# Optimization experiments

Hardware: AMD Instinct MI355X
Metric: run time of the kernel (lower is better)

Reference implementation:

```python
import jax, jax.numpy as jnp
import numpy as np

V, D, H, KV, L, FF, HD = 32000, 768, 12, 4, 4, 2048, 64
N_REP = H // KV  # 3
EPS = 1e-6
ROPE_THETA = 10000.0


def setup_inputs() -> dict:
    key = jax.random.key(0)
    ks = jax.random.split(key, 12)
    s = 0.02
    return {
        'idx': jax.random.randint(ks[0], (1, 2048), 0, V),
        'embed': jax.random.normal(ks[1], (V, D), jnp.float32) * s,
        'ln1_w': jnp.ones((L, D), jnp.float32),
        'Wq': jax.random.normal(ks[2], (L, D, H * HD), jnp.float32) * s,
        'Wk': jax.random.normal(ks[3], (L, D, KV * HD), jnp.float32) * s,
        'Wv': jax.random.normal(ks[4], (L, D, KV * HD), jnp.float32) * s,
        'Wo': jax.random.normal(ks[5], (L, H * HD, D), jnp.float32) * s,
        'ln2_w': jnp.ones((L, D), jnp.float32),
        'Wg': jax.random.normal(ks[6], (L, D, FF), jnp.float32) * s,
        'Wu': jax.random.normal(ks[7], (L, D, FF), jnp.float32) * s,
        'Wd': jax.random.normal(ks[8], (L, FF, D), jnp.float32) * s,
        'normf_w': jnp.ones((D,), jnp.float32),
    }


def _rms(x, w):
    xf = x.astype(jnp.float32)
    var = jnp.mean(xf * xf, axis=-1, keepdims=True)
    return w * (xf * jax.lax.rsqrt(var + EPS)).astype(x.dtype)


def _rotate_half(x):
    x1, x2 = x[..., : x.shape[-1] // 2], x[..., x.shape[-1] // 2:]
    return jnp.concatenate((-x2, x1), axis=-1)


def reference(idx, embed, ln1_w, Wq, Wk, Wv, Wo, ln2_w, Wg, Wu, Wd, normf_w):
    B, T = idx.shape
    x = embed[idx]  # [B,T,D]

    # RoPE tables: cos/sin [1,1,T,HD]
    inv_freq = 1.0 / (ROPE_THETA ** (jnp.arange(0, HD, 2, dtype=jnp.float32) / HD))
    pos = jnp.arange(T, dtype=jnp.float32)
    freqs = pos[:, None] * inv_freq[None, :]          # [T,HD/2]
    emb = jnp.concatenate((freqs, freqs), axis=-1)     # [T,HD]
    cos = jnp.cos(emb)[None, None].astype(x.dtype)
    sin = jnp.sin(emb)[None, None].astype(x.dtype)

    causal = jnp.tril(jnp.ones((T, T), bool))[None, None]  # [1,1,T,T]
    scale = 1.0 / np.sqrt(HD)

    for l in range(L):
        # --- attention ---
        h = _rms(x, ln1_w[l])
        q = (h @ Wq[l]).reshape(B, T, H, HD).transpose(0, 2, 1, 3)   # [B,H,T,HD]
        k = (h @ Wk[l]).reshape(B, T, KV, HD).transpose(0, 2, 1, 3)  # [B,KV,T,HD]
        v = (h @ Wv[l]).reshape(B, T, KV, HD).transpose(0, 2, 1, 3)
        q = q * cos + _rotate_half(q) * sin
        k = k * cos + _rotate_half(k) * sin
        k = jnp.repeat(k, N_REP, axis=1)  # [B,H,T,HD]
        v = jnp.repeat(v, N_REP, axis=1)
        scores = jnp.einsum('bhqd,bhkd->bhqk', q, k) * scale
        scores = jnp.where(causal, scores, -jnp.inf)
        probs = jax.nn.softmax(scores.astype(jnp.float32), axis=-1).astype(q.dtype)
        attn = jnp.einsum('bhqk,bhkd->bhqd', probs, v)
        attn = attn.transpose(0, 2, 1, 3).reshape(B, T, H * HD)
        x = x + attn @ Wo[l]
        # --- gated MLP ---
        h = _rms(x, ln2_w[l])
        x = x + (jax.nn.gelu(h @ Wg[l], approximate=True) * (h @ Wu[l])) @ Wd[l]

    x = _rms(x, normf_w)
    logits = (x @ embed.T).astype(jnp.float32)  # tied lm_head
    return logits
```

## Files before the change

### kernel.cpp

```cpp
#include <hip/hip_runtime.h>

#define TSEQ 2048
#define DM   768
#define NH   12
#define NKV  4
#define HD   64
#define FFD  2048
#define NL   4
#define VOC  32000
#define QKVN 1280

typedef __attribute__((ext_vector_type(8))) short short8;
typedef __attribute__((ext_vector_type(4))) float f32x4;

__device__ __forceinline__ unsigned short f2b(float f) {
  unsigned int u = __float_as_uint(f);
  u += 0x7fffu + ((u >> 16) & 1u);
  return (unsigned short)(u >> 16);
}
__device__ __forceinline__ float b2f(unsigned short u) {
  return __uint_as_float(((unsigned int)u) << 16);
}
__device__ __forceinline__ unsigned int packbf(float a, float b) {
  return (unsigned int)f2b(a) | ((unsigned int)f2b(b) << 16);
}

__device__ __forceinline__ void gl16(const unsigned short* g, unsigned short* l) {
  __builtin_amdgcn_global_load_lds(
      (const __attribute__((address_space(1))) void*)g,
      (__attribute__((address_space(3))) void*)l, 16, 0, 0);
}

__global__ void cast_bf16_kernel(const float* __restrict__ src,
                                 unsigned short* __restrict__ dst, int n4) {
  int i = blockIdx.x * blockDim.x + threadIdx.x;
  if (i >= n4) return;
  float4 v = ((const float4*)src)[i];
  uint2 o; o.x = packbf(v.x, v.y); o.y = packbf(v.z, v.w);
  ((uint2*)dst)[i] = o;
}

__global__ void rope_tab_kernel(float2* __restrict__ tab) {
  int i = blockIdx.x * blockDim.x + threadIdx.x;
  int pos = i >> 5, d = i & 31;
  float inv = exp2f(-(float)d * (13.287712379549449f / 32.0f));
  float sv, cv; sincosf((float)pos * inv, &sv, &cv);
  tab[i] = make_float2(cv, sv);
}

__global__ void transpose_cast_kernel(const float* __restrict__ src,
                                      unsigned short* __restrict__ dst,
                                      int K, int N, size_t sstride, size_t dstride) {
  __shared__ float tile[32][33];
  src += (size_t)blockIdx.z * sstride;
  dst += (size_t)blockIdx.z * dstride;
  int n0 = blockIdx.x * 32, k0 = blockIdx.y * 32;
  int tx = threadIdx.x, ty = threadIdx.y;
  #pragma unroll
  for (int i = 0; i < 4; ++i) {
    int r = ty + i * 8;
    tile[r][tx] = src[(size_t)(k0 + r) * N + n0 + tx];
  }
  __syncthreads();
  #pragma unroll
  for (int i = 0; i < 4; ++i) {
    int r = ty + i * 8;
    dst[(size_t)(n0 + r) * K + k0 + tx] = f2b(tile[tx][r]);
  }
}

__global__ void gather_kernel(const int* __restrict__ idx,
                              const float* __restrict__ embed,
                              float* __restrict__ x) {
  int row = blockIdx.x; int t = threadIdx.x;
  int id = idx[row];
  ((float4*)(x + (size_t)row * DM))[t] = ((const float4*)(embed + (size_t)id * DM))[t];
}

__global__ void rmsnorm_kernel(const float* __restrict__ x,
                               const float* __restrict__ w,
                               unsigned short* __restrict__ out) {
  int row = blockIdx.x; int t = threadIdx.x;
  const float* xr = x + (size_t)row * DM;
  float v0 = xr[t], v1 = xr[t + 256], v2 = xr[t + 512];
  float s = v0*v0 + v1*v1 + v2*v2;
  #pragma unroll
  for (int off = 1; off < 64; off <<= 1) s += __shfl_xor(s, off);
  __shared__ float red[4];
  if ((t & 63) == 0) red[t >> 6] = s;
  __syncthreads();
  float tot = red[0] + red[1] + red[2] + red[3];
  float rs = rsqrtf(tot * (1.0f / DM) + 1e-6f);
  unsigned short* orow = out + (size_t)row * DM;
  orow[t]       = f2b(w[t]       * v0 * rs);
  orow[t + 256] = f2b(w[t + 256] * v1 * rs);
  orow[t + 512] = f2b(w[t + 512] * v2 * rs);
}

__global__ __launch_bounds__(512, 1) void gemm_l8_kernel(
    const unsigned short* __restrict__ A, const unsigned short* __restrict__ Bt,
    float* __restrict__ C, int N, int K) {
  __shared__ unsigned short lds[2][2][256 * 64];
  const int NT = K >> 6;
  int bid = blockIdx.x, nwg = gridDim.x;
  int wgid = (bid & 7) * (nwg >> 3) + (bid >> 3);
  int m0 = (wgid & 7) * 256;
  int n0 = (wgid >> 3) * 256;
  int tid = threadIdx.x;
  int lane = tid & 63, w = tid >> 6;
  int wm = w >> 2, wn = w & 3;
  int al = lane & 15, ag = lane >> 4;
  int swz = (al & 7) << 3;

  int rA = tid >> 3;
  int cK = ((tid & 7) * 8) ^ ((rA & 7) << 3);
  const unsigned short* Ag = A + (size_t)(m0 + rA) * K + cK;
  const unsigned short* Bg = Bt + (size_t)(n0 + rA) * K + cK;

  f32x4 acc[8][4];
  #pragma unroll
  for (int i = 0; i < 8; ++i)
    #pragma unroll
    for (int n = 0; n < 4; ++n) acc[i][n] = (f32x4){0.f, 0.f, 0.f, 0.f};

  #define STAGE(kt, c) { \
    size_t ko = (size_t)(kt) * 64; \
    unsigned short* dA = &lds[(c)][0][0] + w * 512; \
    unsigned short* dB = &lds[(c)][1][0] + w * 512; \
    gl16(Ag + (size_t)0   * K + ko, dA);            \
    gl16(Ag + (size_t)64  * K + ko, dA + 4096);     \
    gl16(Ag + (size_t)128 * K + ko, dA + 8192);     \
    gl16(Ag + (size_t)192 * K + ko, dA + 12288);    \
    gl16(Bg + (size_t)0   * K + ko, dB);            \
    gl16(Bg + (size_t)64  * K + ko, dB + 4096);     \
    gl16(Bg + (size_t)128 * K + ko, dB + 8192);     \
    gl16(Bg + (size_t)192 * K + ko, dB + 12288);    \
  }

  STAGE(0, 0);
  STAGE(1, 1);
  asm volatile("s_waitcnt vmcnt(8)" ::: "memory");
  __builtin_amdgcn_s_barrier();

  for (int t = 0; t < NT; ++t) {
    int cur = t & 1;
    const unsigned short* La = &lds[cur][0][0];
    const unsigned short* Lb = &lds[cur][1][0];
    short8 a0[8], b0[4], a1[8], b1[4];
    #pragma unroll
    for (int i = 0; i < 8; ++i)
      a0[i] = *(const short8*)&La[(wm*128 + i*16 + al)*64 + ((ag*8) ^ swz)];
    #pragma unroll
    for (int n = 0; n < 4; ++n)
      b0[n] = *(const short8*)&Lb[(wn*64 + n*16 + al)*64 + ((ag*8) ^ swz)];
    #pragma unroll
    for (int i = 0; i < 8; ++i)
      #pragma unroll
      for (int n = 0; n < 4; ++n)
        acc[i][n] = __builtin_amdgcn_mfma_f32_16x16x32_bf16(a0[i], b0[n], acc[i][n], 0, 0, 0);
    #pragma unroll
    for (int i = 0; i < 8; ++i)
      a1[i] = *(const short8*)&La[(wm*128 + i*16 + al)*64 + ((32 + ag*8) ^ swz)];
    #pragma unroll
    for (int n = 0; n < 4; ++n)
      b1[n] = *(const short8*)&Lb[(wn*64 + n*16 + al)*64 + ((32 + ag*8) ^ swz)];
    asm volatile("s_waitcnt lgkmcnt(0)" ::: "memory");
    __builtin_amdgcn_s_barrier();
    if (t + 2 < NT) STAGE(t + 2, cur);
    __builtin_amdgcn_s_setprio(1);
    #pragma unroll
    for (int i = 0; i < 8; ++i)
      #pragma unroll
      for (int n = 0; n < 4; ++n)
        acc[i][n] = __builtin_amdgcn_mfma_f32_16x16x32_bf16(a1[i], b1[n], acc[i][n], 0, 0, 0);
    __builtin_amdgcn_s_setprio(0);
    if (t + 2 < NT) { asm volatile("s_waitcnt vmcnt(8)" ::: "memory"); }
    else            { asm volatile("s_waitcnt vmcnt(0)" ::: "memory"); }
    __builtin_amdgcn_s_barrier();
  }
  #undef STAGE

  #pragma unroll
  for (int i = 0; i < 8; ++i)
    #pragma unroll
    for (int r = 0; r < 4; ++r) {
      float* Cr = C + (size_t)(m0 + wm*128 + i*16 + ag*4 + r) * N + n0 + wn*64 + al;
      #pragma unroll
      for (int n = 0; n < 4; ++n) Cr[n * 16] = acc[i][n][r];
    }
}

__global__ __launch_bounds__(512) void gemm_p8_kernel(
    const unsigned short* __restrict__ A, const unsigned short* __restrict__ Bt,
    float* __restrict__ C, int N, int K, int Kc) {
  __shared__ unsigned short lds[2][2][128 * 64];
  const int NT = Kc >> 6;
  int bid = blockIdx.x, nwg = gridDim.x;
  int wgid = (bid & 7) * (nwg >> 3) + (bid >> 3);
  int m0 = (wgid & 15) * 128;
  int n0 = (wgid >> 4) * 128;
  int tid = threadIdx.x;
  int lane = tid & 63, w = tid >> 6;
  int wm = w >> 2, wn = w & 3;
  int al = lane & 15, ag = lane >> 4;
  int swz = (al & 7) << 3;

  size_t koff = (size_t)blockIdx.y * Kc;
  int rp = 8 * w + (lane >> 3);
  int cK = ((lane & 7) * 8) ^ ((lane >> 3) << 3);
  const unsigned short* Ag = A + (size_t)(m0 + rp) * K + koff + cK;
  const unsigned short* Bg = Bt + (size_t)(n0 + rp) * K + koff + cK;

  f32x4 acc[4][2];
  #pragma unroll
  for (int i = 0; i < 4; ++i)
    #pragma unroll
    for (int n = 0; n < 2; ++n) acc[i][n] = (f32x4){0.f, 0.f, 0.f, 0.f};

  #define STAGE(kt, c) { \
    size_t ko = (size_t)(kt) * 64; \
    unsigned short* dA = &lds[(c)][0][0] + w * 512; \
    unsigned short* dB = &lds[(c)][1][0] + w * 512; \
    gl16(Ag + ko,                 dA);        \
    gl16(Ag + (size_t)64*K + ko,  dA + 4096); \
    gl16(Bg + ko,                 dB);        \
    gl16(Bg + (size_t)64*K + ko,  dB + 4096); \
  }

  STAGE(0, 0);
  STAGE(1, 1);
  asm volatile("s_waitcnt vmcnt(4)" ::: "memory");
  __builtin_amdgcn_s_barrier();

  for (int t = 0; t < NT; ++t) {
    int cur = t & 1;
    const unsigned short* La = &lds[cur][0][0];
    const unsigned short* Lb = &lds[cur][1][0];
    short8 a0[4], b0[2], a1[4], b1[2];
    #pragma unroll
    for (int i = 0; i < 4; ++i)
      a0[i] = *(const short8*)&La[(wm*64 + i*16 + al)*64 + ((ag*8) ^ swz)];
    #pragma unroll
    for (int n = 0; n < 2; ++n)
      b0[n] = *(const short8*)&Lb[(wn*32 + n*16 + al)*64 + ((ag*8) ^ swz)];
    #pragma unroll
    for (int i = 0; i < 4; ++i)
      #pragma unroll
      for (int n = 0; n < 2; ++n)
        acc[i][n] = __builtin_amdgcn_mfma_f32_16x16x32_bf16(a0[i], b0[n], acc[i][n], 0, 0, 0);
    #pragma unroll
    for (int i = 0; i < 4; ++i)
      a1[i] = *(const short8*)&La[(wm*64 + i*16 + al)*64 + ((32 + ag*8) ^ swz)];
    #pragma unroll
    for (int n = 0; n < 2; ++n)
      b1[n] = *(const short8*)&Lb[(wn*32 + n*16 + al)*64 + ((32 + ag*8) ^ swz)];
    asm volatile("s_waitcnt lgkmcnt(0)" ::: "memory");
    __builtin_amdgcn_s_barrier();
    if (t + 2 < NT) STAGE(t + 2, cur);
    __builtin_amdgcn_s_setprio(1);
    #pragma unroll
    for (int i = 0; i < 4; ++i)
      #pragma unroll
      for (int n = 0; n < 2; ++n)
        acc[i][n] = __builtin_amdgcn_mfma_f32_16x16x32_bf16(a1[i], b1[n], acc[i][n], 0, 0, 0);
    __builtin_amdgcn_s_setprio(0);
    if (t + 2 < NT) { asm volatile("s_waitcnt vmcnt(4)" ::: "memory"); }
    else            { asm volatile("s_waitcnt vmcnt(0)" ::: "memory"); }
    __builtin_amdgcn_s_barrier();
  }
  #undef STAGE

  #pragma unroll
  for (int i = 0; i < 4; ++i)
    #pragma unroll
    for (int r = 0; r < 4; ++r) {
      float* Cr = C + (size_t)(m0 + wm*64 + i*16 + ag*4 + r) * N + n0 + wn*32 + al;
      #pragma unroll
      for (int n = 0; n < 2; ++n) atomicAdd(&Cr[n * 16], acc[i][n][r]);
    }
}

__device__ __forceinline__ float gelu_t(float x) {
  float x3 = x * x * x;
  return 0.5f * x * (1.0f + tanhf(0.7978845608028654f * (x + 0.044715f * x3)));
}

__global__ __launch_bounds__(512) void gemm_gu8_kernel(
    const unsigned short* __restrict__ A, const unsigned short* __restrict__ BtG,
    const unsigned short* __restrict__ BtU, unsigned short* __restrict__ Cm) {
  __shared__ unsigned short lds[2][3][128 * 64];
  const int K = DM;
  const int NT = K >> 6;
  int bid = blockIdx.x, nwg = gridDim.x;
  int wgid = (bid & 7) * (nwg >> 3) + (bid >> 3);
  int m0 = (wgid & 15) * 128;
  int n0 = (wgid >> 4) * 128;
  int tid = threadIdx.x;
  int lane = tid & 63, w = tid >> 6;
  int wm = w >> 2, wn = w & 3;
  int al = lane & 15, ag = lane >> 4;
  int swz = (al & 7) << 3;

  int rp = 8 * w + (lane >> 3);
  int cK = ((lane & 7) * 8) ^ ((lane >> 3) << 3);
  const unsigned short* Ag = A + (size_t)(m0 + rp) * K + cK;
  const unsigned short* Gg = BtG + (size_t)(n0 + rp) * K + cK;
  const unsigned short* Ug = BtU + (size_t)(n0 + rp) * K + cK;

  f32x4 accg[4][2], accu[4][2];
  #pragma unroll
  for (int i = 0; i < 4; ++i)
    #pragma unroll
    for (int n = 0; n < 2; ++n) {
      accg[i][n] = (f32x4){0.f, 0.f, 0.f, 0.f};
      accu[i][n] = (f32x4){0.f, 0.f, 0.f, 0.f};
    }

  #define STAGE(kt, c) { \
    size_t ko = (size_t)(kt) * 64; \
    unsigned short* dA = &lds[(c)][0][0] + w * 512; \
    unsigned short* dG = &lds[(c)][1][0] + w * 512; \
    unsigned short* dU = &lds[(c)][2][0] + w * 512; \
    gl16(Ag + ko,                 dA);        \
    gl16(Ag + (size_t)64*K + ko,  dA + 4096); \
    gl16(Gg + ko,                 dG);        \
    gl16(Gg + (size_t)64*K + ko,  dG + 4096); \
    gl16(Ug + ko,                 dU);        \
    gl16(Ug + (size_t)64*K + ko,  dU + 4096); \
  }

  STAGE(0, 0);
  STAGE(1, 1);
  asm volatile("s_waitcnt vmcnt(6)" ::: "memory");
  __builtin_amdgcn_s_barrier();

  for (int t = 0; t < NT; ++t) {
    int cur = t & 1;
    const unsigned short* La = &lds[cur][0][0];
    const unsigned short* Lg = &lds[cur][1][0];
    const unsigned short* Lu = &lds[cur][2][0];
    short8 a0[4], g0[2], u0[2], a1[4], g1[2], u1[2];
    #pragma unroll
    for (int i = 0; i < 4; ++i)
      a0[i] = *(const short8*)&La[(wm*64 + i*16 + al)*64 + ((ag*8) ^ swz)];
    #pragma unroll
    for (int n = 0; n < 2; ++n) {
      g0[n] = *(const short8*)&Lg[(wn*32 + n*16 + al)*64 + ((ag*8) ^ swz)];
      u0[n] = *(const short8*)&Lu[(wn*32 + n*16 + al)*64 + ((ag*8) ^ swz)];
    }
    #pragma unroll
    for (int i = 0; i < 4; ++i)
      #pragma unroll
      for (int n = 0; n < 2; ++n) {
        accg[i][n] = __builtin_amdgcn_mfma_f32_16x16x32_bf16(a0[i], g0[n], accg[i][n], 0, 0, 0);
        accu[i][n] = __builtin_amdgcn_mfma_f32_16x16x32_bf16(a0[i], u0[n], accu[i][n], 0, 0, 0);
      }
    #pragma unroll
    for (int i = 0; i < 4; ++i)
      a1[i] = *(const short8*)&La[(wm*64 + i*16 + al)*64 + ((32 + ag*8) ^ swz)];
    #pragma unroll
    for (int n = 0; n < 2; ++n) {
      g1[n] = *(const short8*)&Lg[(wn*32 + n*16 + al)*64 + ((32 + ag*8) ^ swz)];
      u1[n] = *(const short8*)&Lu[(wn*32 + n*16 + al)*64 + ((32 + ag*8) ^ swz)];
    }
    asm volatile("s_waitcnt lgkmcnt(0)" ::: "memory");
    __builtin_amdgcn_s_barrier();
    if (t + 2 < NT) STAGE(t + 2, cur);
    __builtin_amdgcn_s_setprio(1);
    #pragma unroll
    for (int i = 0; i < 4; ++i)
      #pragma unroll
      for (int n = 0; n < 2; ++n) {
        accg[i][n] = __builtin_amdgcn_mfma_f32_16x16x32_bf16(a1[i], g1[n], accg[i][n], 0, 0, 0);
        accu[i][n] = __builtin_amdgcn_mfma_f32_16x16x32_bf16(a1[i], u1[n], accu[i][n], 0, 0, 0);
      }
    __builtin_amdgcn_s_setprio(0);
    if (t + 2 < NT) { asm volatile("s_waitcnt vmcnt(6)" ::: "memory"); }
    else            { asm volatile("s_waitcnt vmcnt(0)" ::: "memory"); }
    __builtin_amdgcn_s_barrier();
  }
  #undef STAGE

  #pragma unroll
  for (int i = 0; i < 4; ++i)
    #pragma unroll
    for (int r = 0; r < 4; ++r) {
      unsigned short* Cr = Cm + (size_t)(m0 + wm*64 + i*16 + ag*4 + r) * FFD + n0 + wn*32 + al;
      #pragma unroll
      for (int n = 0; n < 2; ++n)
        Cr[n * 16] = f2b(gelu_t(accg[i][n][r]) * accu[i][n][r]);
    }
}

__global__ __launch_bounds__(256) void gemm_qkv_kernel(
    const unsigned short* __restrict__ A, const unsigned short* __restrict__ Bt,
    unsigned short* __restrict__ C, unsigned short* __restrict__ vT,
    const float2* __restrict__ rope_tab) {
  const int N = QKVN, K = DM;
  __shared__ unsigned short As[128 * 40];
  __shared__ unsigned short Bs[128 * 40];
  int bid = blockIdx.x, nwg = gridDim.x;
  int wgid = (bid & 7) * (nwg >> 3) + (bid >> 3);
  int m0 = (wgid & 15) * 128;
  int n0 = (wgid >> 4) * 128;
  int tid = threadIdx.x;
  int lane = tid & 63, wave = tid >> 6;
  int wr = (wave >> 1) * 64, wc = (wave & 1) * 64;
  int l16 = lane & 15, lk8 = (lane >> 4) * 8;
  f32x4 acc[4][4];
  #pragma unroll
  for (int m = 0; m < 4; ++m)
    #pragma unroll
    for (int n = 0; n < 4; ++n) acc[m][n] = (f32x4){0.f, 0.f, 0.f, 0.f};
  const unsigned short* Abase = A + (size_t)m0 * K;
  const unsigned short* Bbase = Bt + (size_t)n0 * K;
  int r0 = tid >> 2;
  int c0 = (tid & 3) * 8;
  for (int k0 = 0; k0 < K; k0 += 32) {
    uint4 a0 = *(const uint4*)(Abase + (size_t)r0 * K + k0 + c0);
    uint4 a1 = *(const uint4*)(Abase + (size_t)(r0 + 64) * K + k0 + c0);
    uint4 b0 = *(const uint4*)(Bbase + (size_t)r0 * K + k0 + c0);
    uint4 b1 = *(const uint4*)(Bbase + (size_t)(r0 + 64) * K + k0 + c0);
    *(uint4*)&As[r0 * 40 + c0] = a0;
    *(uint4*)&As[(r0 + 64) * 40 + c0] = a1;
    *(uint4*)&Bs[r0 * 40 + c0] = b0;
    *(uint4*)&Bs[(r0 + 64) * 40 + c0] = b1;
    __syncthreads();
    short8 af[4], bfr[4];
    #pragma unroll
    for (int m = 0; m < 4; ++m) af[m]  = *(const short8*)&As[(wr + m*16 + l16) * 40 + lk8];
    #pragma unroll
    for (int n = 0; n < 4; ++n) bfr[n] = *(const short8*)&Bs[(wc + n*16 + l16) * 40 + lk8];
    #pragma unroll
    for (int m = 0; m < 4; ++m)
      #pragma unroll
      for (int n = 0; n < 4; ++n)
        acc[m][n] = __builtin_amdgcn_mfma_f32_16x16x32_bf16(af[m], bfr[n], acc[m][n], 0, 0, 0);
    __syncthreads();
  }
  bool qk = (n0 + wc) < 1024;
  #pragma unroll
  for (int m = 0; m < 4; ++m)
    #pragma unroll
    for (int r = 0; r < 4; ++r) {
      int pos = m0 + wr + m*16 + ((lane >> 4) << 2) + r;
      if (qk) {
        unsigned short* Cr = C + (size_t)pos * N + n0 + wc + l16;
        #pragma unroll
        for (int n = 0; n < 2; ++n) {
          int d = n * 16 + l16;
          float2 cs = rope_tab[pos * 32 + d];
          float x1 = acc[m][n][r], x2 = acc[m][n + 2][r];
          Cr[n * 16]       = f2b(x1 * cs.x - x2 * cs.y);
          Cr[(n + 2) * 16] = f2b(x2 * cs.x + x1 * cs.y);
        }
      } else {
        #pragma unroll
        for (int n = 0; n < 4; ++n) {
          int hb = n0 + wc + n*16 + l16 - 1024;
          vT[(size_t)hb * TSEQ + pos] = f2b(acc[m][n][r]);
        }
      }
    }
}

__global__ __launch_bounds__(256) void attn_mfma_kernel(
    const unsigned short* __restrict__ qkv, const unsigned short* __restrict__ vT,
    unsigned short* __restrict__ out) {
  __shared__ unsigned short Ks[2][64 * 64];
  __shared__ unsigned short Vt[2][64 * 64];
  __shared__ unsigned short Ps[4][16 * 64];
  int h = blockIdx.y;
  int qt = gridDim.x - 1 - blockIdx.x;
  int r0 = qt * 64;
  int kvh = h / 3;
  int t = threadIdx.x;
  int lane = t & 63, w = t >> 6;
  int l16 = lane & 15, g = lane >> 4;

  int qr = r0 + w * 16 + l16;
  const unsigned short* qrow = qkv + (size_t)qr * QKVN + h * HD;
  short8 aq0 = *(const short8*)(qrow + 8 * g);
  short8 aq1 = *(const short8*)(qrow + 32 + 8 * g);

  int sw = (lane & 7) ^ (lane >> 3);
  int rloc = w * 16 + (lane >> 3);
  const unsigned short* kgb = qkv + (size_t)rloc * QKVN + DM + kvh * HD + 8 * sw;
  const unsigned short* vgb = vT + (size_t)(kvh * 64 + rloc) * TSEQ + 8 * sw;

  #define ASTAGE(kb, c) { \
    unsigned short* kd = &Ks[(c)][0] + w * 1024; \
    unsigned short* vd = &Vt[(c)][0] + w * 1024; \
    gl16(kgb + (size_t)(kb) * QKVN,       kd);       \
    gl16(kgb + (size_t)((kb) + 8) * QKVN, kd + 512); \
    gl16(vgb + (kb),                      vd);       \
    gl16(vgb + (size_t)8 * TSEQ + (kb),   vd + 512); \
  }

  f32x4 o_acc[4];
  float mrun[4], lsum[4];
  #pragma unroll
  for (int i = 0; i < 4; ++i) { o_acc[i] = (f32x4){0.f,0.f,0.f,0.f}; mrun[i] = -1e30f; lsum[i] = 0.f; }

  int nt = qt + 1;
  ASTAGE(0, 0);
  for (int kt = 0; kt < nt; ++kt) {
    int cur = kt & 1;
    int kb = kt * 64;
    if (kt + 1 < nt) {
      ASTAGE((kt + 1) * 64, cur ^ 1);
      asm volatile("s_waitcnt vmcnt(4)" ::: "memory");
    } else {
      asm volatile("s_waitcnt vmcnt(0)" ::: "memory");
    }
    __builtin_amdgcn_s_barrier();

    const unsigned short* Kc = &Ks[cur][0];
    const unsigned short* Vc = &Vt[cur][0];

    f32x4 s_acc[4];
    #pragma unroll
    for (int nb = 0; nb < 4; ++nb) s_acc[nb] = (f32x4){0.f,0.f,0.f,0.f};
    #pragma unroll
    for (int nb = 0; nb < 4; ++nb) {
      int key = nb * 16 + l16;
      short8 bk0 = *(const short8*)&Kc[key * 64 + ((g       ^ (key & 7)) << 3)];
      short8 bk1 = *(const short8*)&Kc[key * 64 + (((4 + g) ^ (key & 7)) << 3)];
      s_acc[nb] = __builtin_amdgcn_mfma_f32_16x16x32_bf16(aq0, bk0, s_acc[nb], 0, 0, 0);
      s_acc[nb] = __builtin_amdgcn_mfma_f32_16x16x32_bf16(aq1, bk1, s_acc[nb], 0, 0, 0);
    }

    bool diag = (kt == qt);
    #pragma unroll
    for (int r = 0; r < 4; ++r) {
      int qg = r0 + w * 16 + g * 4 + r;
      float sv[4];
      #pragma unroll
      for (int nb = 0; nb < 4; ++nb) {
        sv[nb] = s_acc[nb][r] * 0.125f;
        if (diag && (kb + nb * 16 + l16 > qg)) sv[nb] = -1e30f;
      }
      float mx = fmaxf(fmaxf(sv[0], sv[1]), fmaxf(sv[2], sv[3]));
      mx = fmaxf(mx, __shfl_xor(mx, 1));
      mx = fmaxf(mx, __shfl_xor(mx, 2));
      mx = fmaxf(mx, __shfl_xor(mx, 4));
      mx = fmaxf(mx, __shfl_xor(mx, 8));
      if (mx > mrun[r] + 8.0f) {
        float es = __expf(mrun[r] - mx);
        lsum[r] *= es;
        #pragma unroll
        for (int db = 0; db < 4; ++db) o_acc[db][r] *= es;
        mrun[r] = mx;
      }
      float rsum = 0.f;
      #pragma unroll
      for (int nb = 0; nb < 4; ++nb) { sv[nb] = __expf(sv[nb] - mrun[r]); rsum += sv[nb]; }
      lsum[r] += rsum;
      int qloc = g * 4 + r, q7 = qloc & 7;
      #pragma unroll
      for (int nb = 0; nb < 4; ++nb) {
        int key = nb * 16 + l16;
        Ps[w][qloc * 64 + ((((key >> 3) ^ q7) << 3) + (key & 7))] = f2b(sv[nb]);
      }
    }

    #pragma unroll
    for (int kc = 0; kc < 2; ++kc) {
      short8 pa = *(const short8*)&Ps[w][l16 * 64 + (((4 * kc + g) ^ (l16 & 7)) << 3)];
      #pragma unroll
      for (int db = 0; db < 4; ++db) {
        int d = db * 16 + l16;
        short8 bv = *(const short8*)&Vc[d * 64 + (((4 * kc + g) ^ (d & 7)) << 3)];
        o_acc[db] = __builtin_amdgcn_mfma_f32_16x16x32_bf16(pa, bv, o_acc[db], 0, 0, 0);
      }
    }
    __builtin_amdgcn_s_barrier();
  }
  #undef ASTAGE

  #pragma unroll
  for (int r = 0; r < 4; ++r) {
    int qg = r0 + w * 16 + g * 4 + r;
    float s = lsum[r];
    s += __shfl_xor(s, 1);
    s += __shfl_xor(s, 2);
    s += __shfl_xor(s, 4);
    s += __shfl_xor(s, 8);
    float inv = 1.0f / s;
    unsigned short* orow = out + (size_t)qg * DM + h * HD + l16;
    #pragma unroll
    for (int db = 0; db < 4; ++db) orow[db * 16] = f2b(o_acc[db][r] * inv);
  }
}

extern "C" void kernel_launch(void* const* d_in, const int* in_sizes, int n_in,
                              void* d_out, int out_size, void* d_ws, size_t ws_size,
                              hipStream_t stream) {
  const int*   idx   = (const int*)d_in[0];
  const float* embed = (const float*)d_in[1];
  const float* ln1   = (const float*)d_in[2];
  const float* Wq    = (const float*)d_in[3];
  const float* Wk    = (const float*)d_in[4];
  const float* Wv    = (const float*)d_in[5];
  const float* Wo    = (const float*)d_in[6];
  const float* ln2   = (const float*)d_in[7];
  const float* Wg    = (const float*)d_in[8];
  const float* Wu    = (const float*)d_in[9];
  const float* Wd    = (const float*)d_in[10];
  const float* normf = (const float*)d_in[11];
  float* out = (float*)d_out;
  char* ws = (char*)d_ws;
  (void)in_sizes; (void)n_in; (void)out_size; (void)ws_size;

  unsigned short* embed_bf = (unsigned short*)ws;
  size_t off = (size_t)VOC * DM * 2;
  unsigned short* wts = (unsigned short*)(ws + off);
  const size_t LW = (size_t)QKVN * DM + (size_t)DM * DM
                  + 2ull * FFD * DM + (size_t)DM * FFD;
  off += LW * 2ull * NL;
  float* xf = (float*)(ws + off);            off += (size_t)TSEQ * DM * 4;
  unsigned short* h_bf = (unsigned short*)(ws + off);    off += (size_t)TSEQ * DM * 2;
  unsigned short* qkv_bf = (unsigned short*)(ws + off);  off += (size_t)TSEQ * QKVN * 2;
  unsigned short* attn_bf = (unsigned short*)(ws + off); off += (size_t)TSEQ * DM * 2;
  unsigned short* m_bf = (unsigned short*)(ws + off);    off += (size_t)TSEQ * FFD * 2;
  float2* rope_tab = (float2*)(ws + off);    off += (size_t)TSEQ * 32 * 8;
  unsigned short* vT = (unsigned short*)(ws + off);      off += (size_t)NKV * HD * TSEQ * 2;

  cast_bf16_kernel<<<(VOC * DM / 4 + 255) / 256, 256, 0, stream>>>(embed, embed_bf, VOC * DM / 4);
  rope_tab_kernel<<<TSEQ * 32 / 256, 256, 0, stream>>>(rope_tab);

  {
    unsigned short* qkvT = wts;
    unsigned short* woT  = wts + (size_t)QKVN * DM;
    unsigned short* wguT = woT + (size_t)DM * DM;
    unsigned short* wdT  = wguT + 2ull * FFD * DM;
    transpose_cast_kernel<<<dim3(24, 24, NL), dim3(32, 8), 0, stream>>>(Wq, qkvT, 768, 768, 589824, LW);
    transpose_cast_kernel<<<dim3(8, 24, NL),  dim3(32, 8), 0, stream>>>(Wk, qkvT + 768ull * 768, 768, 256, 196608, LW);
    transpose_cast_kernel<<<dim3(8, 24, NL),  dim3(32, 8), 0, stream>>>(Wv, qkvT + 1024ull * 768, 768, 256, 196608, LW);
    transpose_cast_kernel<<<dim3(24, 24, NL), dim3(32, 8), 0, stream>>>(Wo, woT, 768, 768, 589824, LW);
    transpose_cast_kernel<<<dim3(64, 24, NL), dim3(32, 8), 0, stream>>>(Wg, wguT, 768, 2048, 1572864, LW);
    transpose_cast_kernel<<<dim3(64, 24, NL), dim3(32, 8), 0, stream>>>(Wu, wguT + (size_t)FFD * DM, 768, 2048, 1572864, LW);
    transpose_cast_kernel<<<dim3(24, 64, NL), dim3(32, 8), 0, stream>>>(Wd, wdT, 2048, 768, 1572864, LW);
  }

  gather_kernel<<<TSEQ, 192, 0, stream>>>(idx, embed, xf);

  for (int l = 0; l < NL; ++l) {
    unsigned short* base = wts + (size_t)l * LW;
    unsigned short* qkvT = base;
    unsigned short* woT  = base + (size_t)QKVN * DM;
    unsigned short* wguT = woT + (size_t)DM * DM;
    unsigned short* wdT  = wguT + 2ull * FFD * DM;

    rmsnorm_kernel<<<TSEQ, 256, 0, stream>>>(xf, ln1 + (size_t)l * DM, h_bf);
    gemm_qkv_kernel<<<(QKVN / 128) * 16, 256, 0, stream>>>(h_bf, qkvT, qkv_bf, vT, rope_tab);
    attn_mfma_kernel<<<dim3(TSEQ / 64, NH), 256, 0, stream>>>(qkv_bf, vT, attn_bf);
    gemm_p8_kernel<<<dim3((DM / 128) * 16, 3), 512, 0, stream>>>(attn_bf, woT, xf, DM, DM, 256);
    rmsnorm_kernel<<<TSEQ, 256, 0, stream>>>(xf, ln2 + (size_t)l * DM, h_bf);
    gemm_gu8_kernel<<<(FFD / 128) * 16, 512, 0, stream>>>(h_bf, wguT, wguT + (size_t)FFD * DM, m_bf);
    gemm_p8_kernel<<<dim3((DM / 128) * 16, 4), 512, 0, stream>>>(m_bf, wdT, xf, DM, FFD, 512);
  }

  rmsnorm_kernel<<<TSEQ, 256, 0, stream>>>(xf, normf, h_bf);
  gemm_l8_kernel<<<(VOC / 256) * (TSEQ / 256), 512, 0, stream>>>(h_bf, embed_bf, out, VOC, DM);
}
```

Measured before the change: 852.5 us.

## Split causal attention KV range into chunks with a separate combine kernel

Causal attention q-tiles are split into up to four KV chunks of eight tiles each, so long rows are processed by several blocks in parallel. Partial unnormalized outputs and running max/sum are written to fp32 scratch, which aliases the MLP buffer. A new combine kernel rescales and merges them into bf16. This targets load imbalance and low block count in the triangular attention workload, at the cost of an extra launch and fp32 partial traffic.

Result: faster. 769.8 us (-9.7%).

```diff
diff --git a/kernel.cpp b/kernel.cpp
--- a/kernel.cpp
+++ b/kernel.cpp
@@ -464,14 +464,22 @@
     }
 }
 
-__global__ __launch_bounds__(256) void attn_mfma_kernel(
+__global__ __launch_bounds__(256) void attn_chunk_kernel(
     const unsigned short* __restrict__ qkv, const unsigned short* __restrict__ vT,
-    unsigned short* __restrict__ out) {
+    unsigned short* __restrict__ out, float* __restrict__ pO, float* __restrict__ pML) {
   __shared__ unsigned short Ks[2][64 * 64];
   __shared__ unsigned short Vt[2][64 * 64];
   __shared__ unsigned short Ps[4][16 * 64];
-  int h = blockIdx.y;
-  int qt = gridDim.x - 1 - blockIdx.x;
+  int s = blockIdx.x, h = blockIdx.y;
+  int qt, ci;
+  if (s < 8)       { qt = s;                ci = 0; }
+  else if (s < 24) { qt = 8 + ((s-8) >> 1); ci = (s-8) & 1; }
+  else if (s < 48) { qt = 16 + (s-24) / 3;  ci = (s-24) % 3; }
+  else             { qt = 24 + ((s-48) >> 2); ci = (s-48) & 3; }
+  int nt = qt + 1;
+  int t0 = ci * 8;
+  int t1 = t0 + 8; if (t1 > nt) t1 = nt;
+  int cnt = (nt + 7) >> 3;
   int r0 = qt * 64;
   int kvh = h / 3;
   int t = threadIdx.x;
@@ -502,12 +510,11 @@
   #pragma unroll
   for (int i = 0; i < 4; ++i) { o_acc[i] = (f32x4){0.f,0.f,0.f,0.f}; mrun[i] = -1e30f; lsum[i] = 0.f; }
 
-  int nt = qt + 1;
-  ASTAGE(0, 0);
-  for (int kt = 0; kt < nt; ++kt) {
-    int cur = kt & 1;
+  ASTAGE(t0 * 64, 0);
+  for (int kt = t0; kt < t1; ++kt) {
+    int cur = (kt - t0) & 1;
     int kb = kt * 64;
-    if (kt + 1 < nt) {
+    if (kt + 1 < t1) {
       ASTAGE((kt + 1) * 64, cur ^ 1);
       asm volatile("s_waitcnt vmcnt(4)" ::: "memory");
     } else {
@@ -578,19 +585,80 @@
   }
   #undef ASTAGE
 
-  #pragma unroll
-  for (int r = 0; r < 4; ++r) {
-    int qg = r0 + w * 16 + g * 4 + r;
-    float s = lsum[r];
-    s += __shfl_xor(s, 1);
-    s += __shfl_xor(s, 2);
-    s += __shfl_xor(s, 4);
-    s += __shfl_xor(s, 8);
-    float inv = 1.0f / s;
-    unsigned short* orow = out + (size_t)qg * DM + h * HD + l16;
-    #pragma unroll
-    for (int db = 0; db < 4; ++db) orow[db * 16] = f2b(o_acc[db][r] * inv);
-  }
+  if (cnt == 1) {
+    #pragma unroll
+    for (int r = 0; r < 4; ++r) {
+      int qg = r0 + w * 16 + g * 4 + r;
+      float sr = lsum[r];
+      sr += __shfl_xor(sr, 1);
+      sr += __shfl_xor(sr, 2);
+      sr += __shfl_xor(sr, 4);
+      sr += __shfl_xor(sr, 8);
+      float inv = 1.0f / sr;
+      unsigned short* orow = out + (size_t)qg * DM + h * HD + l16;
+      #pragma unroll
+      for (int db = 0; db < 4; ++db) orow[db * 16] = f2b(o_acc[db][r] * inv);
+    }
+  } else {
+    size_t slotg = (size_t)h * 80 + s;
+    float* po = pO + slotg * 4096;
+    float* pm = pML + slotg * 128;
+    #pragma unroll
+    for (int r = 0; r < 4; ++r) {
+      int row = w * 16 + g * 4 + r;
+      float sr = lsum[r];
+      sr += __shfl_xor(sr, 1);
+      sr += __shfl_xor(sr, 2);
+      sr += __shfl_xor(sr, 4);
+      sr += __shfl_xor(sr, 8);
+      #pragma unroll
+      for (int db = 0; db < 4; ++db) po[row * 64 + db * 16 + l16] = o_acc[db][r];
+      if (l16 == 0) { pm[row * 2] = mrun[r]; pm[row * 2 + 1] = sr; }
+    }
+  }
+}
+
+__global__ __launch_bounds__(256) void attn_combine_kernel(
+    const float* __restrict__ pO, const float* __restrict__ pML,
+    unsigned short* __restrict__ out) {
+  int h = blockIdx.y;
+  int qt = 8 + blockIdx.x;
+  int base, cnt;
+  if (qt < 16)      { base = 8 + (qt - 8) * 2;  cnt = 2; }
+  else if (qt < 24) { base = 24 + (qt - 16) * 3; cnt = 3; }
+  else              { base = 48 + (qt - 24) * 4; cnt = 4; }
+  int t = threadIdx.x;
+  int row = t >> 2, d0 = (t & 3) * 16;
+  float m[4], l[4];
+  float M = -1e30f;
+  for (int c = 0; c < cnt; ++c) {
+    const float* pm = pML + ((size_t)h * 80 + base + c) * 128 + row * 2;
+    m[c] = pm[0]; l[c] = pm[1];
+    M = fmaxf(M, m[c]);
+  }
+  float o[16];
+  #pragma unroll
+  for (int j = 0; j < 16; ++j) o[j] = 0.f;
+  float wl = 0.f;
+  for (int c = 0; c < cnt; ++c) {
+    float wc = __expf(m[c] - M);
+    wl += wc * l[c];
+    const float4* po = (const float4*)(pO + ((size_t)h * 80 + base + c) * 4096 + row * 64 + d0);
+    #pragma unroll
+    for (int q = 0; q < 4; ++q) {
+      float4 v = po[q];
+      o[q*4+0] += wc * v.x; o[q*4+1] += wc * v.y;
+      o[q*4+2] += wc * v.z; o[q*4+3] += wc * v.w;
+    }
+  }
+  float inv = 1.0f / wl;
+  unsigned short* orow = out + (size_t)(qt * 64 + row) * DM + h * HD + d0;
+  uint4 s0, s1;
+  s0.x = packbf(o[0]*inv,  o[1]*inv);  s0.y = packbf(o[2]*inv,  o[3]*inv);
+  s0.z = packbf(o[4]*inv,  o[5]*inv);  s0.w = packbf(o[6]*inv,  o[7]*inv);
+  s1.x = packbf(o[8]*inv,  o[9]*inv);  s1.y = packbf(o[10]*inv, o[11]*inv);
+  s1.z = packbf(o[12]*inv, o[13]*inv); s1.w = packbf(o[14]*inv, o[15]*inv);
+  ((uint4*)orow)[0] = s0; ((uint4*)orow)[1] = s1;
 }
 
 extern "C" void kernel_launch(void* const* d_in, const int* in_sizes, int n_in,
@@ -622,7 +690,10 @@
   unsigned short* h_bf = (unsigned short*)(ws + off);    off += (size_t)TSEQ * DM * 2;
   unsigned short* qkv_bf = (unsigned short*)(ws + off);  off += (size_t)TSEQ * QKVN * 2;
   unsigned short* attn_bf = (unsigned short*)(ws + off); off += (size_t)TSEQ * DM * 2;
-  unsigned short* m_bf = (unsigned short*)(ws + off);    off += (size_t)TSEQ * FFD * 2;
+  float* pO = (float*)(ws + off);
+  unsigned short* m_bf = (unsigned short*)(ws + off);
+  off += (size_t)NH * 80 * 4096 * 4;
+  float* pML = (float*)(ws + off);           off += (size_t)NH * 80 * 128 * 4;
   float2* rope_tab = (float2*)(ws + off);    off += (size_t)TSEQ * 32 * 8;
   unsigned short* vT = (unsigned short*)(ws + off);      off += (size_t)NKV * HD * TSEQ * 2;
 
@@ -654,7 +725,8 @@
 
     rmsnorm_kernel<<<TSEQ, 256, 0, stream>>>(xf, ln1 + (size_t)l * DM, h_bf);
     gemm_qkv_kernel<<<(QKVN / 128) * 16, 256, 0, stream>>>(h_bf, qkvT, qkv_bf, vT, rope_tab);
-    attn_mfma_kernel<<<dim3(TSEQ / 64, NH), 256, 0, stream>>>(qkv_bf, vT, attn_bf);
+    attn_chunk_kernel<<<dim3(80, NH), 256, 0, stream>>>(qkv_bf, vT, attn_bf, pO, pML);
+    attn_combine_kernel<<<dim3(24, NH), 256, 0, stream>>>(pO, pML, attn_bf);
     gemm_p8_kernel<<<dim3((DM / 128) * 16, 3), 512, 0, stream>>>(attn_bf, woT, xf, DM, DM, 256);
     rmsnorm_kernel<<<TSEQ, 256, 0, stream>>>(xf, ln2 + (size_t)l * DM, h_bf);
     gemm_gu8_kernel<<<(FFD / 128) * 16, 512, 0, stream>>>(h_bf, wguT, wguT + (size_t)FFD * DM, m_bf);
```
